# Optimization experiments

Hardware: AMD Instinct MI355X
Metric: run time of the kernel (lower is better)

Reference implementation:

```python
import jax, jax.numpy as jnp
import numpy as np

B, S, D, H, K, L, NS, NT = 32, 512, 1024, 512, 16, 16, 16, 16
SMOOTH = 0.1
EPS = 1e-8


def setup_inputs() -> dict:
    key = jax.random.key(0)
    ks = jax.random.split(key, 16)
    hidden_layers = jax.random.normal(ks[0], (B, S, D), jnp.float32)
    span_start = jax.random.randint(ks[1], (B, K), 0, S - L).astype(jnp.int32)
    span_idx = span_start[..., None] + jnp.arange(L, dtype=jnp.int32)  # [B,K,L] in-range
    span_mask = jnp.ones((B, K, L), jnp.float32)
    span_end = span_start + (L - 1)
    length = jnp.full((B,), S, jnp.int32)
    slot_emb = jax.random.normal(ks[2], (B, K, D), jnp.float32)
    tgt_slot_embs = jax.random.normal(ks[3], (NT, D), jnp.float32)
    src_slot_ids = jax.random.randint(ks[4], (B, K), 0, NS).astype(jnp.int32)
    sc = 0.02
    p = {
        'Wih_f': jax.random.normal(ks[5], (4 * H, D)) * sc,
        'Whh_f': jax.random.normal(ks[6], (4 * H, H)) * sc,
        'bih_f': jnp.zeros((4 * H,)), 'bhh_f': jnp.zeros((4 * H,)),
        'Wih_b': jax.random.normal(ks[7], (4 * H, D)) * sc,
        'Whh_b': jax.random.normal(ks[8], (4 * H, H)) * sc,
        'bih_b': jnp.zeros((4 * H,)), 'bhh_b': jnp.zeros((4 * H,)),
        # slot_name_projection_for_slot / _for_context are eye-initialized with zero bias
        'Wps1': jnp.eye(D), 'bps1': jnp.zeros((D,)),
        'Wps2': jnp.eye(D), 'bps2': jnp.zeros((D,)),
        'Wpc1': jnp.eye(D), 'bpc1': jnp.zeros((D,)),
        'Wpc2': jnp.eye(D), 'bpc2': jnp.zeros((D,)),
    }
    inp = dict(hidden_layers=hidden_layers, span_idx=span_idx, span_mask=span_mask,
               span_start=span_start, span_end=span_end, length=length,
               slot_emb=slot_emb, tgt_slot_embs=tgt_slot_embs, src_slot_ids=src_slot_ids)
    inp.update(p)
    return inp


def _lstm_dir(x, m, Wih, Whh, bih, bhh):
    # x: [N,L,D], m: [N,L]; masked steps carry state through, emit 0
    N = x.shape[0]
    h0 = jnp.zeros((N, H), x.dtype)
    c0 = jnp.zeros((N, H), x.dtype)

    def step(carry, xm):
        h, c = carry
        xt, mt = xm
        g = xt @ Wih.T + h @ Whh.T + (bih + bhh)
        i, f, gg, o = jnp.split(g, 4, axis=-1)  # torch gate order i,f,g,o
        cn = jax.nn.sigmoid(f) * c + jax.nn.sigmoid(i) * jnp.tanh(gg)
        hn = jax.nn.sigmoid(o) * jnp.tanh(cn)
        mt = mt[:, None]
        h = mt * hn + (1.0 - mt) * h
        c = mt * cn + (1.0 - mt) * c
        return (h, c), h * mt

    _, ys = jax.lax.scan(step, (h0, c0), (jnp.swapaxes(x, 0, 1), m.T))
    return jnp.swapaxes(ys, 0, 1)  # [N,L,H]


def _mlp(x, W1, b1, W2, b2):
    # Linear -> Tanh -> (Dropout eval=identity) -> Linear
    return jnp.tanh(x @ W1.T + b1) @ W2.T + b2


def reference(hidden_layers, span_idx, span_mask, span_start, span_end, length,
              slot_emb, tgt_slot_embs, src_slot_ids,
              Wih_f, Whh_f, bih_f, bhh_f, Wih_b, Whh_b, bih_b, bhh_b,
              Wps1, bps1, Wps2, bps2, Wpc1, bpc1, Wpc2, bpc2):
    # gather span tokens: [B,K,L,D]
    spans = hidden_layers[jnp.arange(B)[:, None, None], span_idx]
    x = spans.reshape(B * K, L, D)
    m = span_mask.reshape(B * K, L)
    hf = _lstm_dir(x, m, Wih_f, Whh_f, bih_f, bhh_f)
    hb = _lstm_dir(x[:, ::-1], m[:, ::-1], Wih_b, Whh_b, bih_b, bhh_b)[:, ::-1]
    out = jnp.concatenate([hf, hb], axis=-1)           # [BK,L,2H]
    slot_feats = out.sum(axis=1).reshape(B, K, 2 * H)  # sum-pool over span

    # context attention (faithful to source: returns attn @ hidden, no softmax)
    sf = jax.lax.stop_gradient(slot_feats)
    pos = jnp.arange(S)
    cmask = (pos[None, None, :] < span_start[..., None]) | \
            ((pos[None, None, :] > span_end[..., None]) & (pos[None, None, :] < length[:, None, None]))
    attn = jnp.einsum('bkd,bsd->bks', sf, hidden_layers) * cmask.astype(hidden_layers.dtype)
    context = jnp.einsum('bks,bsd->bkd', attn, hidden_layers)  # [B,K,D]

    # smooth labels via projected slot-name embeddings (all detached in source)
    s_cat = jnp.concatenate([_mlp(slot_emb, Wps1, bps1, Wps2, bps2),
                             _mlp(slot_emb, Wpc1, bpc1, Wpc2, bpc2)], axis=-1)  # [B,K,2D]
    t_cat = jnp.concatenate([_mlp(tgt_slot_embs, Wps1, bps1, Wps2, bps2),
                             _mlp(tgt_slot_embs, Wpc1, bpc1, Wpc2, bpc2)], axis=-1)  # [NT,2D]
    s_cat = jax.lax.stop_gradient(s_cat)
    t_cat = jax.lax.stop_gradient(t_cat)
    sn = jnp.maximum(jnp.linalg.norm(s_cat, axis=-1), EPS)
    tn = jnp.maximum(jnp.linalg.norm(t_cat, axis=-1), EPS)
    sim = jnp.einsum('bkd,td->bkt', s_cat, t_cat) / (sn[..., None] * tn[None, None, :])
    sim = sim / sim.sum(axis=-1, keepdims=True) * (1.0 - SMOOTH)
    one_hot = jax.nn.one_hot(src_slot_ids, NS, dtype=sim.dtype) * SMOOTH
    labels = jnp.concatenate([one_hot, sim], axis=-1)  # [B,K,NS+NT]

    return jnp.concatenate([slot_feats, context, labels], axis=-1)  # [B,K,2H+D+NS+NT]
```

## Files before the change

kernel.cpp:

```cpp
#include <hip/hip_runtime.h>
#include <cstdio>

#define B_ 32
#define S_ 512
#define D_ 1024
#define H_ 512
#define K_ 16
#define L_ 16
#define NT_ 16
#define NSEQ 512
#define XROWS 8192
#define G4H 2048
#define OUTC 2080
#define MROWS 528

typedef unsigned short u16;
typedef __bf16 bf16x8 __attribute__((ext_vector_type(8)));
typedef float f32x4 __attribute__((ext_vector_type(4)));

__device__ inline u16 f2b(float f) {
  union { float f; unsigned u; } x; x.f = f;
  unsigned r = x.u + 0x7FFFu + ((x.u >> 16) & 1u);
  return (u16)(r >> 16);
}
__device__ inline float b2f(u16 h) {
  union { unsigned u; float f; } c; c.u = ((unsigned)h) << 16;
  return c.f;
}
__device__ inline float sigf(float x) { return 1.0f / (1.0f + expf(-x)); }
__device__ inline float wredsum(float v) {
#pragma unroll
  for (int off = 32; off > 0; off >>= 1) v += __shfl_xor(v, off);
  return v;
}
__device__ inline void gl16(const u16* g, u16* l) {
  __builtin_amdgcn_global_load_lds(
      (const __attribute__((address_space(1))) unsigned int*)g,
      (__attribute__((address_space(3))) unsigned int*)l, 16, 0, 0);
}

__global__ __launch_bounds__(256) void split_kernel(const float* __restrict__ in,
                                                    u16* __restrict__ hi,
                                                    u16* __restrict__ lo, int n) {
  int i = blockIdx.x * 256 + threadIdx.x;
  if (i >= n) return;
  float x = in[i];
  u16 h = f2b(x);
  hi[i] = h;
  lo[i] = f2b(x - b2f(h));
}

__global__ __launch_bounds__(256) void hsplit_kernel(const float* __restrict__ in,
                                                     u16* __restrict__ hi,
                                                     u16* __restrict__ lo) {
  size_t i = ((size_t)blockIdx.x * 256 + threadIdx.x) * 4;
  float4 v = *reinterpret_cast<const float4*>(in + i);
  float a[4] = {v.x, v.y, v.z, v.w};
#pragma unroll
  for (int j = 0; j < 4; ++j) {
    u16 h = f2b(a[j]);
    hi[i + j] = h;
    lo[i + j] = f2b(a[j] - b2f(h));
  }
}

__global__ __launch_bounds__(256) void icast_kernel(const float* __restrict__ W,
                                                    u16* __restrict__ out, int Kd) {
  int rp = blockIdx.x;
  int j = rp >> 2, g = rp & 3;
  const float* src = W + ((size_t)(g * H_ + j)) * Kd;
  u16* dst = out + (size_t)rp * Kd;
  for (int k = threadIdx.x; k < Kd; k += 256) dst[k] = f2b(src[k]);
}

__global__ __launch_bounds__(256) void bsum_kernel(const float* __restrict__ bih,
                                                   const float* __restrict__ bhh,
                                                   float* __restrict__ bsum) {
  int rp = blockIdx.x * 256 + threadIdx.x;
  if (rp >= G4H) return;
  int j = rp >> 2, g = rp & 3;
  bsum[rp] = bih[g * H_ + j] + bhh[g * H_ + j];
}

__global__ __launch_bounds__(256) void big_gemm_kernel(
    const u16* __restrict__ Hh, const int* __restrict__ span_idx,
    const u16* __restrict__ Wih2, u16* __restrict__ G2) {
  __shared__ u16 As[128 * 32];
  __shared__ u16 Bs[128 * 32];
  const int tid = threadIdx.x;
  const int bn = blockIdx.x * 128, bm = blockIdx.y * 128;
  const int wave = tid >> 6, lane = tid & 63;
  const int wm = (wave >> 1) * 64, wn = (wave & 1) * 64;
  const int fr = lane & 15;
  const int kg = (lane >> 4) * 8;

  const u16* asrc[2];
  const u16* bsrc[2];
  u16* adst[2];
  u16* bdst[2];
#pragma unroll
  for (int j = 0; j < 2; ++j) {
    int c = tid + 256 * j;
    int gr = bm + (c >> 2);
    int b = gr >> 8;
    int sidx = span_idx[gr];
    asrc[j] = Hh + ((size_t)(b * S_ + sidx)) * D_ + (c & 3) * 8;
    bsrc[j] = Wih2 + (size_t)(bn + (c >> 2)) * D_ + (c & 3) * 8;
    int ub = (wave * 64 + 256 * j) * 8;
    adst[j] = As + ub;
    bdst[j] = Bs + ub;
  }

  f32x4 acc[4][4] = {};
  for (int k0 = 0; k0 < D_; k0 += 32) {
    gl16(asrc[0] + k0, adst[0]);
    gl16(asrc[1] + k0, adst[1]);
    gl16(bsrc[0] + k0, bdst[0]);
    gl16(bsrc[1] + k0, bdst[1]);
    __syncthreads();
    bf16x8 af[4], bfr[4];
#pragma unroll
    for (int m = 0; m < 4; ++m)
      af[m] = *reinterpret_cast<const bf16x8*>(&As[(wm + m * 16 + fr) * 32 + kg]);
#pragma unroll
    for (int n = 0; n < 4; ++n)
      bfr[n] = *reinterpret_cast<const bf16x8*>(&Bs[(wn + n * 16 + fr) * 32 + kg]);
#pragma unroll
    for (int m = 0; m < 4; ++m)
#pragma unroll
      for (int n = 0; n < 4; ++n)
        acc[m][n] = __builtin_amdgcn_mfma_f32_16x16x32_bf16(af[m], bfr[n], acc[m][n], 0, 0, 0);
    __syncthreads();
  }
  const int ci = lane & 15;
  const int r0 = (lane >> 4) * 4;
#pragma unroll
  for (int m = 0; m < 4; ++m)
#pragma unroll
    for (int n = 0; n < 4; ++n) {
      int col = bn + wn + n * 16 + ci;
#pragma unroll
      for (int r = 0; r < 4; ++r) {
        int row = bm + wm + m * 16 + r0 + r;
        G2[(size_t)row * 4096 + col] = f2b(acc[m][n][r]);
      }
    }
}

__global__ __launch_bounds__(256) void lstm_step_kernel(
    const u16* __restrict__ hbf_in,
    const u16* __restrict__ Whhf, const u16* __restrict__ Whhb,
    const u16* __restrict__ G2,
    const float* __restrict__ bsumf, const float* __restrict__ bsumb,
    const float* __restrict__ mask,
    float* __restrict__ hst, float* __restrict__ cst,
    u16* __restrict__ hbf_out,
    float* __restrict__ sf,
    int t, int first) {
  __shared__ u16 As[64 * 32];
  __shared__ u16 Bs[64 * 32];
  const int tid = threadIdx.x;
  const int bz = blockIdx.z;
  const int treal = bz ? (L_ - 1 - t) : t;
  const u16* Whh = bz ? Whhb : Whhf;
  const float* bsum = bz ? bsumb : bsumf;
  const size_t sofs = (size_t)bz * NSEQ * H_;
  const int bm = blockIdx.y * 64, bn = blockIdx.x * 64;
  const int wave = tid >> 6, lane = tid & 63;
  const int wm = (wave >> 1) * 32, wn = (wave & 1) * 32;
  f32x4 acc[2][2] = {};
  const int fr = lane & 15;
  const int kg = (lane >> 4) * 8;

  if (!first) {
    const int c = tid;
    const u16* asrc = hbf_in + sofs + (size_t)(bm + (c >> 2)) * H_ + (c & 3) * 8;
    const u16* bsrc = Whh + (size_t)(bn + (c >> 2)) * H_ + (c & 3) * 8;
    u16* adst = As + wave * 512;
    u16* bdst = Bs + wave * 512;
    for (int k0 = 0; k0 < H_; k0 += 32) {
      gl16(asrc + k0, adst);
      gl16(bsrc + k0, bdst);
      __syncthreads();
      bf16x8 af[2], bfr[2];
#pragma unroll
      for (int m = 0; m < 2; ++m)
        af[m] = *reinterpret_cast<const bf16x8*>(&As[(wm + m * 16 + fr) * 32 + kg]);
#pragma unroll
      for (int n = 0; n < 2; ++n)
        bfr[n] = *reinterpret_cast<const bf16x8*>(&Bs[(wn + n * 16 + fr) * 32 + kg]);
#pragma unroll
      for (int m = 0; m < 2; ++m)
#pragma unroll
        for (int n = 0; n < 2; ++n)
          acc[m][n] = __builtin_amdgcn_mfma_f32_16x16x32_bf16(af[m], bfr[n], acc[m][n], 0, 0, 0);
      __syncthreads();
    }
  }

  const int ci = lane & 15;
  const int r0 = (lane >> 4) * 4;
  const int q = lane & 3;
#pragma unroll
  for (int m = 0; m < 2; ++m)
#pragma unroll
    for (int n = 0; n < 2; ++n) {
      int c = bn + wn + n * 16 + ci;
      int rowbase = bm + wm + m * 16 + r0;
      float val[4];
#pragma unroll
      for (int r = 0; r < 4; ++r) {
        int nrow = rowbase + r;
        float g2 = b2f(G2[((size_t)nrow * L_ + treal) * 4096 + (size_t)bz * 2048 + c]);
        val[r] = acc[m][n][r] + g2 + bsum[c];
      }
      float x1[4], x2[4], x3[4];
#pragma unroll
      for (int r = 0; r < 4; ++r) {
        x1[r] = __shfl_xor(val[r], 1);
        x2[r] = __shfl_xor(val[r], 2);
        x3[r] = __shfl_xor(x1[r], 2);
      }
      if (q == 0) {
        int j = c >> 2;
#pragma unroll
        for (int r = 0; r < 4; ++r) {
          int nrow = rowbase + r;
          float gi = val[r], gf = x1[r], gg = x2[r], go = x3[r];
          float mv = mask[nrow * L_ + treal];
          size_t sidx = sofs + (size_t)nrow * H_ + j;
          float co = first ? 0.f : cst[sidx];
          float ho = first ? 0.f : hst[sidx];
          float cn = sigf(gf) * co + sigf(gi) * tanhf(gg);
          float hn = sigf(go) * tanhf(cn);
          float hnew = mv * hn + (1.f - mv) * ho;
          float cnew = mv * cn + (1.f - mv) * co;
          hst[sidx] = hnew;
          cst[sidx] = cnew;
          hbf_out[sidx] = f2b(hnew);
          size_t fidx = (size_t)nrow * 1024 + bz * 512 + j;
          float contrib = hnew * mv;
          if (first) sf[fidx] = contrib;
          else sf[fidx] += contrib;
        }
      }
    }
}

__global__ __launch_bounds__(256) void copy_sf_split_kernel(const float* __restrict__ sf,
                                                            float* __restrict__ out,
                                                            u16* __restrict__ sfh,
                                                            u16* __restrict__ sfl) {
  int bk = blockIdx.x;
  for (int d = threadIdx.x; d < 1024; d += 256) {
    size_t i = (size_t)bk * 1024 + d;
    float v = sf[i];
    out[(size_t)bk * OUTC + d] = v;
    u16 h = f2b(v);
    sfh[i] = h;
    sfl[i] = f2b(v - b2f(h));
  }
}

__global__ __launch_bounds__(256) void attn_mfma_kernel(
    const u16* __restrict__ sfh, const u16* __restrict__ sfl,
    const u16* __restrict__ Hh, const u16* __restrict__ Hl,
    const int* __restrict__ sstart, const int* __restrict__ send,
    const int* __restrict__ len,
    u16* __restrict__ attn_h, u16* __restrict__ attn_l) {
  __shared__ u16 Bh[128 * 32];
  __shared__ u16 Bl[128 * 32];
  const int b = blockIdx.x;
  const int s0 = blockIdx.y * 128;
  const int tid = threadIdx.x;
  const int wave = tid >> 6, lane = tid & 63;
  const int fr = lane & 15;
  const int kg = (lane >> 4) * 8;
  f32x4 acc[2] = {};

  const u16* hsrc[2];
  const u16* lsrc[2];
  u16* hdst[2];
  u16* ldst[2];
#pragma unroll
  for (int j = 0; j < 2; ++j) {
    int c = tid + 256 * j;
    size_t goff = ((size_t)b * S_ + s0 + (c >> 2)) * D_ + (c & 3) * 8;
    hsrc[j] = Hh + goff;
    lsrc[j] = Hl + goff;
    int ub = (wave * 64 + 256 * j) * 8;
    hdst[j] = Bh + ub;
    ldst[j] = Bl + ub;
  }

  for (int k0 = 0; k0 < D_; k0 += 32) {
    gl16(hsrc[0] + k0, hdst[0]);
    gl16(hsrc[1] + k0, hdst[1]);
    gl16(lsrc[0] + k0, ldst[0]);
    gl16(lsrc[1] + k0, ldst[1]);
    __syncthreads();
    size_t aoff = ((size_t)b * 16 + fr) * D_ + k0 + kg;
    bf16x8 ah = *reinterpret_cast<const bf16x8*>(sfh + aoff);
    bf16x8 al = *reinterpret_cast<const bf16x8*>(sfl + aoff);
#pragma unroll
    for (int nt = 0; nt < 2; ++nt) {
      bf16x8 bh = *reinterpret_cast<const bf16x8*>(&Bh[(wave * 32 + nt * 16 + fr) * 32 + kg]);
      bf16x8 bl = *reinterpret_cast<const bf16x8*>(&Bl[(wave * 32 + nt * 16 + fr) * 32 + kg]);
      acc[nt] = __builtin_amdgcn_mfma_f32_16x16x32_bf16(ah, bh, acc[nt], 0, 0, 0);
      acc[nt] = __builtin_amdgcn_mfma_f32_16x16x32_bf16(ah, bl, acc[nt], 0, 0, 0);
      acc[nt] = __builtin_amdgcn_mfma_f32_16x16x32_bf16(al, bh, acc[nt], 0, 0, 0);
    }
    __syncthreads();
  }
  const int ln = len[b];
#pragma unroll
  for (int nt = 0; nt < 2; ++nt) {
    int s = s0 + wave * 32 + nt * 16 + (lane & 15);
#pragma unroll
    for (int r = 0; r < 4; ++r) {
      int krow = (lane >> 4) * 4 + r;
      int bk = b * 16 + krow;
      int st = sstart[bk], en = send[bk];
      bool cm = (s < st) || ((s > en) && (s < ln));
      float v = cm ? acc[nt][r] : 0.f;
      u16 h = f2b(v);
      size_t idx = (size_t)bk * S_ + s;
      attn_h[idx] = h;
      attn_l[idx] = f2b(v - b2f(h));
    }
  }
}

__global__ __launch_bounds__(256) void ctx_mfma_kernel(
    const u16* __restrict__ attn_h, const u16* __restrict__ attn_l,
    const u16* __restrict__ Hh, const u16* __restrict__ Hl,
    float* __restrict__ out) {
  __shared__ u16 Th[128][34];
  __shared__ u16 Tl[128][34];
  const int b = blockIdx.x;
  const int d0 = blockIdx.y * 128;
  const int tid = threadIdx.x;
  const int wave = tid >> 6, lane = tid & 63;
  const int fr = lane & 15;
  const int kg = (lane >> 4) * 8;
  f32x4 acc[2] = {};

  for (int k0 = 0; k0 < S_; k0 += 32) {
#pragma unroll
    for (int pass = 0; pass < 2; ++pass) {
      int idx = pass * 256 + tid;
      int srow = idx >> 4;
      int dch = (idx & 15) * 8;
      size_t goff = ((size_t)b * S_ + k0 + srow) * D_ + d0 + dch;
      uint4 vh = *reinterpret_cast<const uint4*>(Hh + goff);
      uint4 vl = *reinterpret_cast<const uint4*>(Hl + goff);
      const u16* ph = reinterpret_cast<const u16*>(&vh);
      const u16* pl = reinterpret_cast<const u16*>(&vl);
#pragma unroll
      for (int i = 0; i < 8; ++i) {
        Th[dch + i][srow] = ph[i];
        Tl[dch + i][srow] = pl[i];
      }
    }
    __syncthreads();
    size_t aoff = ((size_t)b * 16 + fr) * S_ + k0 + kg;
    bf16x8 ah = *reinterpret_cast<const bf16x8*>(attn_h + aoff);
    bf16x8 al = *reinterpret_cast<const bf16x8*>(attn_l + aoff);
#pragma unroll
    for (int nt = 0; nt < 2; ++nt) {
      bf16x8 bh = *reinterpret_cast<const bf16x8*>(&Th[wave * 32 + nt * 16 + fr][kg]);
      bf16x8 bl = *reinterpret_cast<const bf16x8*>(&Tl[wave * 32 + nt * 16 + fr][kg]);
      acc[nt] = __builtin_amdgcn_mfma_f32_16x16x32_bf16(ah, bh, acc[nt], 0, 0, 0);
      acc[nt] = __builtin_amdgcn_mfma_f32_16x16x32_bf16(ah, bl, acc[nt], 0, 0, 0);
      acc[nt] = __builtin_amdgcn_mfma_f32_16x16x32_bf16(al, bh, acc[nt], 0, 0, 0);
    }
    __syncthreads();
  }
#pragma unroll
  for (int nt = 0; nt < 2; ++nt) {
    int d = d0 + wave * 32 + nt * 16 + (lane & 15);
#pragma unroll
    for (int r = 0; r < 4; ++r) {
      int krow = (lane >> 4) * 4 + r;
      out[((size_t)b * 16 + krow) * OUTC + 1024 + d] = acc[nt][r];
    }
  }
}

__global__ __launch_bounds__(256) void mlp_gemm_kernel(
    const u16* __restrict__ Ah, const u16* __restrict__ Al, int a_br_stride,
    const u16* __restrict__ B0h, const u16* __restrict__ B0l,
    const u16* __restrict__ B1h, const u16* __restrict__ B1l,
    float* __restrict__ P, int M) {
  __shared__ u16 Ash[64 * 32];
  __shared__ u16 Asl[64 * 32];
  __shared__ u16 Bsh[64 * 32];
  __shared__ u16 Bsl[64 * 32];
  const int tid = threadIdx.x;
  const int zz = blockIdx.z;
  const int br = zz >> 2, ks = zz & 3;
  const u16* Ah_ = Ah + (size_t)br * a_br_stride;
  const u16* Al_ = Al + (size_t)br * a_br_stride;
  const u16* Bh = br ? B1h : B0h;
  const u16* Bl = br ? B1l : B0l;
  const int bm = blockIdx.y * 64, bn = blockIdx.x * 64;
  const int wave = tid >> 6, lane = tid & 63;
  const int wm = (wave >> 1) * 32, wn = (wave & 1) * 32;
  f32x4 acc[2][2] = {};
  const int fr = lane & 15;
  const int kg = (lane >> 4) * 8;

  const int c = tid;
  int ga = bm + (c >> 2);
  if (ga >= M) ga = M - 1;
  const u16* ahsrc = Ah_ + (size_t)ga * D_ + (c & 3) * 8;
  const u16* alsrc = Al_ + (size_t)ga * D_ + (c & 3) * 8;
  const u16* bhsrc = Bh + (size_t)(bn + (c >> 2)) * D_ + (c & 3) * 8;
  const u16* blsrc = Bl + (size_t)(bn + (c >> 2)) * D_ + (c & 3) * 8;
  u16* d0 = Ash + wave * 512;
  u16* d1 = Asl + wave * 512;
  u16* d2 = Bsh + wave * 512;
  u16* d3 = Bsl + wave * 512;

  const int kbeg = ks * 256;
  for (int k0 = kbeg; k0 < kbeg + 256; k0 += 32) {
    gl16(ahsrc + k0, d0);
    gl16(alsrc + k0, d1);
    gl16(bhsrc + k0, d2);
    gl16(blsrc + k0, d3);
    __syncthreads();
    bf16x8 afh[2], afl[2], bfh[2], bfl[2];
#pragma unroll
    for (int m = 0; m < 2; ++m) {
      afh[m] = *reinterpret_cast<const bf16x8*>(&Ash[(wm + m * 16 + fr) * 32 + kg]);
      afl[m] = *reinterpret_cast<const bf16x8*>(&Asl[(wm + m * 16 + fr) * 32 + kg]);
    }
#pragma unroll
    for (int n = 0; n < 2; ++n) {
      bfh[n] = *reinterpret_cast<const bf16x8*>(&Bsh[(wn + n * 16 + fr) * 32 + kg]);
      bfl[n] = *reinterpret_cast<const bf16x8*>(&Bsl[(wn + n * 16 + fr) * 32 + kg]);
    }
#pragma unroll
    for (int m = 0; m < 2; ++m)
#pragma unroll
      for (int n = 0; n < 2; ++n) {
        acc[m][n] = __builtin_amdgcn_mfma_f32_16x16x32_bf16(afh[m], bfh[n], acc[m][n], 0, 0, 0);
        acc[m][n] = __builtin_amdgcn_mfma_f32_16x16x32_bf16(afh[m], bfl[n], acc[m][n], 0, 0, 0);
        acc[m][n] = __builtin_amdgcn_mfma_f32_16x16x32_bf16(afl[m], bfh[n], acc[m][n], 0, 0, 0);
      }
    __syncthreads();
  }
  const int ci = lane & 15;
  const int r0 = (lane >> 4) * 4;
#pragma unroll
  for (int m = 0; m < 2; ++m)
#pragma unroll
    for (int n = 0; n < 2; ++n) {
      int col = bn + wn + n * 16 + ci;
#pragma unroll
      for (int r = 0; r < 4; ++r) {
        int row = bm + wm + m * 16 + r0 + r;
        if (row < M)
          P[((size_t)zz * MROWS + row) * D_ + col] = acc[m][n][r];
      }
    }
}

__global__ __launch_bounds__(256) void mlp_reduce_kernel(
    const float* __restrict__ P,
    const float* __restrict__ bias0, const float* __restrict__ bias1,
    u16* __restrict__ Oh, u16* __restrict__ Ol,
    float* __restrict__ Cf,
    int mode) {
  int i = blockIdx.x * 256 + threadIdx.x;
  int e = i * 4;
  const int per_br = MROWS * D_;
  int br = e / per_br;
  int rem = e - br * per_br;
  int row = rem >> 10;
  int col = rem & 1023;
  float4 s = {0.f, 0.f, 0.f, 0.f};
#pragma unroll
  for (int ks = 0; ks < 4; ++ks) {
    float4 v = *reinterpret_cast<const float4*>(
        P + ((size_t)(br * 4 + ks) * MROWS + row) * D_ + col);
    s.x += v.x; s.y += v.y; s.z += v.z; s.w += v.w;
  }
  const float* bias = br ? bias1 : bias0;
  s.x += bias[col]; s.y += bias[col + 1]; s.z += bias[col + 2]; s.w += bias[col + 3];
  if (mode == 0) {
    float a[4] = {tanhf(s.x), tanhf(s.y), tanhf(s.z), tanhf(s.w)};
    size_t o = (size_t)br * per_br + (size_t)row * D_ + col;
#pragma unroll
    for (int j = 0; j < 4; ++j) {
      u16 h = f2b(a[j]);
      Oh[o + j] = h;
      Ol[o + j] = f2b(a[j] - b2f(h));
    }
  } else {
    *reinterpret_cast<float4*>(Cf + (size_t)row * 2048 + br * 1024 + col) = s;
  }
}

__global__ __launch_bounds__(64) void labels_kernel(
    const float* __restrict__ s_cat, const float* __restrict__ t_cat,
    const int* __restrict__ src_ids, float* __restrict__ out) {
  int bk = blockIdx.x, lane = threadIdx.x;
  const float* srow = s_cat + (size_t)bk * 2048;
  float np = 0.f;
  float dots[16], tsq[16];
#pragma unroll
  for (int t = 0; t < 16; ++t) { dots[t] = 0.f; tsq[t] = 0.f; }
  for (int j = lane; j < 2048; j += 64) {
    float sv = srow[j];
    np += sv * sv;
#pragma unroll
    for (int t = 0; t < 16; ++t) {
      float tv = t_cat[t * 2048 + j];
      dots[t] += sv * tv;
      tsq[t] += tv * tv;
    }
  }
  np = wredsum(np);
#pragma unroll
  for (int t = 0; t < 16; ++t) { dots[t] = wredsum(dots[t]); tsq[t] = wredsum(tsq[t]); }
  float sn = fmaxf(sqrtf(np), 1e-8f);
  float ssum = 0.f;
  float sims[16];
#pragma unroll
  for (int t = 0; t < 16; ++t) {
    float tn = fmaxf(sqrtf(tsq[t]), 1e-8f);
    sims[t] = dots[t] / (sn * tn);
    ssum += sims[t];
  }
  float scale = 0.9f / ssum;
  if (lane < 16) {
    out[(size_t)bk * OUTC + 2064 + lane] = sims[lane] * scale;
  } else if (lane < 32) {
    int t2 = lane - 16;
    out[(size_t)bk * OUTC + 2048 + t2] = (src_ids[bk] == t2) ? 0.1f : 0.f;
  }
}

extern "C" void kernel_launch(void* const* d_in, const int* in_sizes, int n_in,
                              void* d_out, int out_size, void* d_ws, size_t ws_size,
                              hipStream_t stream) {
  const float* hidden    = (const float*)d_in[0];
  const int*   span_idx  = (const int*)d_in[1];
  const float* span_mask = (const float*)d_in[2];
  const int*   span_start= (const int*)d_in[3];
  const int*   span_end  = (const int*)d_in[4];
  const int*   length    = (const int*)d_in[5];
  const float* slot_emb  = (const float*)d_in[6];
  const float* tgt       = (const float*)d_in[7];
  const int*   src_ids   = (const int*)d_in[8];
  const float* Wih_f = (const float*)d_in[9];
  const float* Whh_f = (const float*)d_in[10];
  const float* bih_f = (const float*)d_in[11];
  const float* bhh_f = (const float*)d_in[12];
  const float* Wih_b = (const float*)d_in[13];
  const float* Whh_b = (const float*)d_in[14];
  const float* bih_b = (const float*)d_in[15];
  const float* bhh_b = (const float*)d_in[16];
  const float* Wps1 = (const float*)d_in[17];
  const float* bps1 = (const float*)d_in[18];
  const float* Wps2 = (const float*)d_in[19];
  const float* bps2 = (const float*)d_in[20];
  const float* Wpc1 = (const float*)d_in[21];
  const float* bpc1 = (const float*)d_in[22];
  const float* Wpc2 = (const float*)d_in[23];
  const float* bpc2 = (const float*)d_in[24];
  float* out = (float*)d_out;

  char* p = (char*)d_ws;
  auto alloc = [&](size_t bytes) -> void* {
    void* r = (void*)p;
    p += (bytes + 255) & ~(size_t)255;
    return r;
  };
  char*  BIG1  = (char*)alloc((size_t)XROWS * 4096 * 2);
  char*  BIG2  = (char*)alloc((size_t)2 * B_ * S_ * D_ * 2);
  float* hst   = (float*)alloc((size_t)2 * NSEQ * H_ * 4);
  float* cst   = (float*)alloc((size_t)2 * NSEQ * H_ * 4);
  u16*   hbfA  = (u16*)alloc((size_t)2 * NSEQ * H_ * 2);
  u16*   hbfB  = (u16*)alloc((size_t)2 * NSEQ * H_ * 2);
  float* sf    = (float*)alloc((size_t)NSEQ * 1024 * 4);
  u16*   sfh   = (u16*)alloc((size_t)NSEQ * 1024 * 2);
  u16*   sfl   = (u16*)alloc((size_t)NSEQ * 1024 * 2);
  u16*   attn_h= (u16*)alloc((size_t)NSEQ * S_ * 2);
  u16*   attn_l= (u16*)alloc((size_t)NSEQ * S_ * 2);
  float* CAT   = (float*)alloc((size_t)MROWS * 2048 * 4);
  u16* Wih2_i = (u16*)alloc((size_t)2 * G4H * D_ * 2);
  u16* Whhf_i = (u16*)alloc((size_t)G4H * H_ * 2);
  u16* Whhb_i = (u16*)alloc((size_t)G4H * H_ * 2);
  float* bsumf = (float*)alloc(G4H * 4);
  float* bsumb = (float*)alloc(G4H * 4);
  u16* W1sh = (u16*)alloc((size_t)D_ * D_ * 2); u16* W1sl = (u16*)alloc((size_t)D_ * D_ * 2);
  u16* W2sh = (u16*)alloc((size_t)D_ * D_ * 2); u16* W2sl = (u16*)alloc((size_t)D_ * D_ * 2);
  u16* W1ch = (u16*)alloc((size_t)D_ * D_ * 2); u16* W1cl = (u16*)alloc((size_t)D_ * D_ * 2);
  u16* W2ch = (u16*)alloc((size_t)D_ * D_ * 2); u16* W2cl = (u16*)alloc((size_t)D_ * D_ * 2);
  u16* SEh = (u16*)alloc((size_t)MROWS * D_ * 2); u16* SEl = (u16*)alloc((size_t)MROWS * D_ * 2);
  u16* T1h = (u16*)alloc((size_t)2 * MROWS * D_ * 2);
  u16* T1l = (u16*)alloc((size_t)2 * MROWS * D_ * 2);

  u16*   G2 = (u16*)BIG1;
  float* P  = (float*)BIG1;
  u16*   Hh = (u16*)BIG2;
  u16*   Hl = Hh + (size_t)B_ * S_ * D_;

  size_t need = (size_t)(p - (char*)d_ws);
  if (need > ws_size) {
    fprintf(stderr, "kernel_launch: ws too small, need %zu have %zu\n", need, ws_size);
    return;
  }

  auto split = [&](const float* src, u16* hi, u16* lo, int n) {
    split_kernel<<<(n + 255) / 256, 256, 0, stream>>>(src, hi, lo, n);
  };

  icast_kernel<<<G4H, 256, 0, stream>>>(Wih_f, Wih2_i, D_);
  icast_kernel<<<G4H, 256, 0, stream>>>(Wih_b, Wih2_i + (size_t)G4H * D_, D_);
  icast_kernel<<<G4H, 256, 0, stream>>>(Whh_f, Whhf_i, H_);
  icast_kernel<<<G4H, 256, 0, stream>>>(Whh_b, Whhb_i, H_);
  bsum_kernel<<<8, 256, 0, stream>>>(bih_f, bhh_f, bsumf);
  bsum_kernel<<<8, 256, 0, stream>>>(bih_b, bhh_b, bsumb);
  split(Wps1, W1sh, W1sl, D_ * D_);
  split(Wps2, W2sh, W2sl, D_ * D_);
  split(Wpc1, W1ch, W1cl, D_ * D_);
  split(Wpc2, W2ch, W2cl, D_ * D_);
  split(slot_emb, SEh, SEl, NSEQ * D_);
  split(tgt, SEh + (size_t)NSEQ * D_, SEl + (size_t)NSEQ * D_, NT_ * D_);

  hsplit_kernel<<<(B_ * S_ * D_) / (4 * 256), 256, 0, stream>>>(hidden, Hh, Hl);

  {
    dim3 g(4096 / 128, XROWS / 128);
    big_gemm_kernel<<<g, 256, 0, stream>>>(Hh, span_idx, Wih2_i, G2);
  }

  for (int t = 0; t < L_; ++t) {
    const u16* hin = (t & 1) ? hbfA : hbfB;
    u16* hout = (t & 1) ? hbfB : hbfA;
    dim3 g(G4H / 64, NSEQ / 64, 2);
    lstm_step_kernel<<<g, 256, 0, stream>>>(hin, Whhf_i, Whhb_i, G2, bsumf, bsumb,
                                            span_mask, hst, cst, hout, sf,
                                            t, t == 0 ? 1 : 0);
  }

  copy_sf_split_kernel<<<NSEQ, 256, 0, stream>>>(sf, out, sfh, sfl);

  {
    dim3 g(B_, S_ / 128);
    attn_mfma_kernel<<<g, 256, 0, stream>>>(sfh, sfl, Hh, Hl,
                                            span_start, span_end, length,
                                            attn_h, attn_l);
  }
  {
    dim3 g(B_, D_ / 128);
    ctx_mfma_kernel<<<g, 256, 0, stream>>>(attn_h, attn_l, Hh, Hl, out);
  }

  {
    dim3 g(D_ / 64, (MROWS + 63) / 64, 8);
    dim3 rg((2 * MROWS * D_) / (4 * 256));
    mlp_gemm_kernel<<<g, 256, 0, stream>>>(SEh, SEl, 0, W1sh, W1sl, W1ch, W1cl, P, MROWS);
    mlp_reduce_kernel<<<rg, 256, 0, stream>>>(P, bps1, bpc1, T1h, T1l, nullptr, 0);
    mlp_gemm_kernel<<<g, 256, 0, stream>>>(T1h, T1l, MROWS * D_, W2sh, W2sl, W2ch, W2cl, P, MROWS);
    mlp_reduce_kernel<<<rg, 256, 0, stream>>>(P, bps2, bpc2, nullptr, nullptr, CAT, 1);
  }

  const float* t_cat = CAT + (size_t)NSEQ * 2048;
  labels_kernel<<<NSEQ, 64, 0, stream>>>(CAT, t_cat, src_ids, out);
}
```

Baseline: 633.2 us.

## Double-buffer GEMM staging with swizzled LDS, relayout G2, fp32 context kernel

The big input GEMM, the LSTM recurrent step and the MLP GEMM now use double-buffered LDS staging. The next K-tile's global-to-LDS loads are issued before waiting on the current one, and raw barriers replace __syncthreads. LDS tiles use an XOR swizzle to reduce bank conflicts. G2 is stored time-major so each LSTM step reads a contiguous slab. The split-bf16 MFMA context GEMM is replaced by a plain fp32 FMA kernel reading attention weights written as fp32, which drops the transposed LDS staging and the three-pass bf16 emulation but gives up MFMA throughput.

Result: no change. 644.3 us (+1.7%).

```diff
diff --git a/kernel.cpp b/kernel.cpp
--- a/kernel.cpp
+++ b/kernel.cpp
@@ -39,6 +39,16 @@
       (__attribute__((address_space(3))) unsigned int*)l, 16, 0, 0);
 }
 
+__device__ inline int swzidx(int R, int c) {
+  return (R >> 1) * 64 + (((((R & 1) << 2) | c) ^ ((R >> 1) & 7)) << 3);
+}
+__device__ inline void stage_map(int wave, int lane, int j, int& lrow, int& cu) {
+  int sr = j * 32 + wave * 8 + (lane >> 3);
+  int ci = (lane & 7) ^ (sr & 7);
+  lrow = sr * 2 + (ci >> 2);
+  cu = (ci & 3) * 8;
+}
+
 __global__ __launch_bounds__(256) void split_kernel(const float* __restrict__ in,
                                                     u16* __restrict__ hi,
                                                     u16* __restrict__ lo, int n) {
@@ -85,52 +95,64 @@
 __global__ __launch_bounds__(256) void big_gemm_kernel(
     const u16* __restrict__ Hh, const int* __restrict__ span_idx,
     const u16* __restrict__ Wih2, u16* __restrict__ G2) {
-  __shared__ u16 As[128 * 32];
-  __shared__ u16 Bs[128 * 32];
+  __shared__ u16 As[2][128 * 32];
+  __shared__ u16 Bs[2][128 * 32];
   const int tid = threadIdx.x;
   const int bn = blockIdx.x * 128, bm = blockIdx.y * 128;
   const int wave = tid >> 6, lane = tid & 63;
   const int wm = (wave >> 1) * 64, wn = (wave & 1) * 64;
   const int fr = lane & 15;
-  const int kg = (lane >> 4) * 8;
+  const int cc = lane >> 4;
 
   const u16* asrc[2];
   const u16* bsrc[2];
-  u16* adst[2];
-  u16* bdst[2];
+  int doff[2];
 #pragma unroll
   for (int j = 0; j < 2; ++j) {
-    int c = tid + 256 * j;
-    int gr = bm + (c >> 2);
+    int lrow, cu;
+    stage_map(wave, lane, j, lrow, cu);
+    int gr = bm + lrow;
     int b = gr >> 8;
     int sidx = span_idx[gr];
-    asrc[j] = Hh + ((size_t)(b * S_ + sidx)) * D_ + (c & 3) * 8;
-    bsrc[j] = Wih2 + (size_t)(bn + (c >> 2)) * D_ + (c & 3) * 8;
-    int ub = (wave * 64 + 256 * j) * 8;
-    adst[j] = As + ub;
-    bdst[j] = Bs + ub;
-  }
+    asrc[j] = Hh + ((size_t)(b * S_ + sidx)) * D_ + cu;
+    bsrc[j] = Wih2 + (size_t)(bn + lrow) * D_ + cu;
+    doff[j] = (j * 256 + wave * 64) * 8;
+  }
+  int aoff[4], boff[4];
+#pragma unroll
+  for (int m = 0; m < 4; ++m) aoff[m] = swzidx(wm + m * 16 + fr, cc);
+#pragma unroll
+  for (int n = 0; n < 4; ++n) boff[n] = swzidx(wn + n * 16 + fr, cc);
 
   f32x4 acc[4][4] = {};
+  auto STAGE = [&](int buf, int k0) {
+    gl16(asrc[0] + k0, &As[buf][doff[0]]);
+    gl16(asrc[1] + k0, &As[buf][doff[1]]);
+    gl16(bsrc[0] + k0, &Bs[buf][doff[0]]);
+    gl16(bsrc[1] + k0, &Bs[buf][doff[1]]);
+  };
+  STAGE(0, 0);
+  int cur = 0;
   for (int k0 = 0; k0 < D_; k0 += 32) {
-    gl16(asrc[0] + k0, adst[0]);
-    gl16(asrc[1] + k0, adst[1]);
-    gl16(bsrc[0] + k0, bdst[0]);
-    gl16(bsrc[1] + k0, bdst[1]);
-    __syncthreads();
+    if (k0 + 32 < D_) {
+      STAGE(cur ^ 1, k0 + 32);
+      asm volatile("s_waitcnt vmcnt(4)" ::: "memory");
+    } else {
+      asm volatile("s_waitcnt vmcnt(0)" ::: "memory");
+    }
+    __builtin_amdgcn_s_barrier();
     bf16x8 af[4], bfr[4];
 #pragma unroll
-    for (int m = 0; m < 4; ++m)
-      af[m] = *reinterpret_cast<const bf16x8*>(&As[(wm + m * 16 + fr) * 32 + kg]);
-#pragma unroll
-    for (int n = 0; n < 4; ++n)
-      bfr[n] = *reinterpret_cast<const bf16x8*>(&Bs[(wn + n * 16 + fr) * 32 + kg]);
+    for (int m = 0; m < 4; ++m) af[m] = *reinterpret_cast<const bf16x8*>(&As[cur][aoff[m]]);
+#pragma unroll
+    for (int n = 0; n < 4; ++n) bfr[n] = *reinterpret_cast<const bf16x8*>(&Bs[cur][boff[n]]);
 #pragma unroll
     for (int m = 0; m < 4; ++m)
 #pragma unroll
       for (int n = 0; n < 4; ++n)
         acc[m][n] = __builtin_amdgcn_mfma_f32_16x16x32_bf16(af[m], bfr[n], acc[m][n], 0, 0, 0);
-    __syncthreads();
+    __builtin_amdgcn_s_barrier();
+    cur ^= 1;
   }
   const int ci = lane & 15;
   const int r0 = (lane >> 4) * 4;
@@ -142,7 +164,8 @@
 #pragma unroll
       for (int r = 0; r < 4; ++r) {
         int row = bm + wm + m * 16 + r0 + r;
-        G2[(size_t)row * 4096 + col] = f2b(acc[m][n][r]);
+        size_t g2row = (size_t)(row & 15) * NSEQ + (row >> 4);
+        G2[g2row * 4096 + col] = f2b(acc[m][n][r]);
       }
     }
 }
@@ -157,8 +180,8 @@
     u16* __restrict__ hbf_out,
     float* __restrict__ sf,
     int t, int first) {
-  __shared__ u16 As[64 * 32];
-  __shared__ u16 Bs[64 * 32];
+  __shared__ u16 As[2][64 * 32];
+  __shared__ u16 Bs[2][64 * 32];
   const int tid = threadIdx.x;
   const int bz = blockIdx.z;
   const int treal = bz ? (L_ - 1 - t) : t;
@@ -170,31 +193,46 @@
   const int wm = (wave >> 1) * 32, wn = (wave & 1) * 32;
   f32x4 acc[2][2] = {};
   const int fr = lane & 15;
-  const int kg = (lane >> 4) * 8;
+  const int cc = lane >> 4;
 
   if (!first) {
-    const int c = tid;
-    const u16* asrc = hbf_in + sofs + (size_t)(bm + (c >> 2)) * H_ + (c & 3) * 8;
-    const u16* bsrc = Whh + (size_t)(bn + (c >> 2)) * H_ + (c & 3) * 8;
-    u16* adst = As + wave * 512;
-    u16* bdst = Bs + wave * 512;
+    int lrow, cu;
+    stage_map(wave, lane, 0, lrow, cu);
+    const u16* asrc = hbf_in + sofs + (size_t)(bm + lrow) * H_ + cu;
+    const u16* bsrc = Whh + (size_t)(bn + lrow) * H_ + cu;
+    const int doff = wave * 64 * 8;
+    int aoff[2], boff[2];
+#pragma unroll
+    for (int m = 0; m < 2; ++m) aoff[m] = swzidx(wm + m * 16 + fr, cc);
+#pragma unroll
+    for (int n = 0; n < 2; ++n) boff[n] = swzidx(wn + n * 16 + fr, cc);
+
+    auto STAGE = [&](int buf, int k0) {
+      gl16(asrc + k0, &As[buf][doff]);
+      gl16(bsrc + k0, &Bs[buf][doff]);
+    };
+    STAGE(0, 0);
+    int cur = 0;
     for (int k0 = 0; k0 < H_; k0 += 32) {
-      gl16(asrc + k0, adst);
-      gl16(bsrc + k0, bdst);
-      __syncthreads();
+      if (k0 + 32 < H_) {
+        STAGE(cur ^ 1, k0 + 32);
+        asm volatile("s_waitcnt vmcnt(2)" ::: "memory");
+      } else {
+        asm volatile("s_waitcnt vmcnt(0)" ::: "memory");
+      }
+      __builtin_amdgcn_s_barrier();
       bf16x8 af[2], bfr[2];
 #pragma unroll
-      for (int m = 0; m < 2; ++m)
-        af[m] = *reinterpret_cast<const bf16x8*>(&As[(wm + m * 16 + fr) * 32 + kg]);
-#pragma unroll
-      for (int n = 0; n < 2; ++n)
-        bfr[n] = *reinterpret_cast<const bf16x8*>(&Bs[(wn + n * 16 + fr) * 32 + kg]);
+      for (int m = 0; m < 2; ++m) af[m] = *reinterpret_cast<const bf16x8*>(&As[cur][aoff[m]]);
+#pragma unroll
+      for (int n = 0; n < 2; ++n) bfr[n] = *reinterpret_cast<const bf16x8*>(&Bs[cur][boff[n]]);
 #pragma unroll
       for (int m = 0; m < 2; ++m)
 #pragma unroll
         for (int n = 0; n < 2; ++n)
           acc[m][n] = __builtin_amdgcn_mfma_f32_16x16x32_bf16(af[m], bfr[n], acc[m][n], 0, 0, 0);
-      __syncthreads();
+      __builtin_amdgcn_s_barrier();
+      cur ^= 1;
     }
   }
 
@@ -211,7 +249,7 @@
 #pragma unroll
       for (int r = 0; r < 4; ++r) {
         int nrow = rowbase + r;
-        float g2 = b2f(G2[((size_t)nrow * L_ + treal) * 4096 + (size_t)bz * 2048 + c]);
+        float g2 = b2f(G2[((size_t)treal * NSEQ + nrow) * 4096 + (size_t)bz * 2048 + c]);
         val[r] = acc[m][n][r] + g2 + bsum[c];
       }
       float x1[4], x2[4], x3[4];
@@ -267,7 +305,7 @@
     const u16* __restrict__ Hh, const u16* __restrict__ Hl,
     const int* __restrict__ sstart, const int* __restrict__ send,
     const int* __restrict__ len,
-    u16* __restrict__ attn_h, u16* __restrict__ attn_l) {
+    float* __restrict__ attn_f) {
   __shared__ u16 Bh[128 * 32];
   __shared__ u16 Bl[128 * 32];
   const int b = blockIdx.x;
@@ -275,37 +313,39 @@
   const int tid = threadIdx.x;
   const int wave = tid >> 6, lane = tid & 63;
   const int fr = lane & 15;
-  const int kg = (lane >> 4) * 8;
+  const int cc = lane >> 4;
+  const int kg = cc * 8;
   f32x4 acc[2] = {};
 
   const u16* hsrc[2];
   const u16* lsrc[2];
-  u16* hdst[2];
-  u16* ldst[2];
+  int doff[2];
 #pragma unroll
   for (int j = 0; j < 2; ++j) {
-    int c = tid + 256 * j;
-    size_t goff = ((size_t)b * S_ + s0 + (c >> 2)) * D_ + (c & 3) * 8;
+    int lrow, cu;
+    stage_map(wave, lane, j, lrow, cu);
+    size_t goff = ((size_t)b * S_ + s0 + lrow) * D_ + cu;
     hsrc[j] = Hh + goff;
     lsrc[j] = Hl + goff;
-    int ub = (wave * 64 + 256 * j) * 8;
-    hdst[j] = Bh + ub;
-    ldst[j] = Bl + ub;
-  }
+    doff[j] = (j * 256 + wave * 64) * 8;
+  }
+  int boff[2];
+#pragma unroll
+  for (int nt = 0; nt < 2; ++nt) boff[nt] = swzidx(wave * 32 + nt * 16 + fr, cc);
 
   for (int k0 = 0; k0 < D_; k0 += 32) {
-    gl16(hsrc[0] + k0, hdst[0]);
-    gl16(hsrc[1] + k0, hdst[1]);
-    gl16(lsrc[0] + k0, ldst[0]);
-    gl16(lsrc[1] + k0, ldst[1]);
+    gl16(hsrc[0] + k0, &Bh[doff[0]]);
+    gl16(hsrc[1] + k0, &Bh[doff[1]]);
+    gl16(lsrc[0] + k0, &Bl[doff[0]]);
+    gl16(lsrc[1] + k0, &Bl[doff[1]]);
     __syncthreads();
     size_t aoff = ((size_t)b * 16 + fr) * D_ + k0 + kg;
     bf16x8 ah = *reinterpret_cast<const bf16x8*>(sfh + aoff);
     bf16x8 al = *reinterpret_cast<const bf16x8*>(sfl + aoff);
 #pragma unroll
     for (int nt = 0; nt < 2; ++nt) {
-      bf16x8 bh = *reinterpret_cast<const bf16x8*>(&Bh[(wave * 32 + nt * 16 + fr) * 32 + kg]);
-      bf16x8 bl = *reinterpret_cast<const bf16x8*>(&Bl[(wave * 32 + nt * 16 + fr) * 32 + kg]);
+      bf16x8 bh = *reinterpret_cast<const bf16x8*>(&Bh[boff[nt]]);
+      bf16x8 bl = *reinterpret_cast<const bf16x8*>(&Bl[boff[nt]]);
       acc[nt] = __builtin_amdgcn_mfma_f32_16x16x32_bf16(ah, bh, acc[nt], 0, 0, 0);
       acc[nt] = __builtin_amdgcn_mfma_f32_16x16x32_bf16(ah, bl, acc[nt], 0, 0, 0);
       acc[nt] = __builtin_amdgcn_mfma_f32_16x16x32_bf16(al, bh, acc[nt], 0, 0, 0);
@@ -322,68 +362,41 @@
       int bk = b * 16 + krow;
       int st = sstart[bk], en = send[bk];
       bool cm = (s < st) || ((s > en) && (s < ln));
-      float v = cm ? acc[nt][r] : 0.f;
-      u16 h = f2b(v);
-      size_t idx = (size_t)bk * S_ + s;
-      attn_h[idx] = h;
-      attn_l[idx] = f2b(v - b2f(h));
-    }
-  }
-}
-
-__global__ __launch_bounds__(256) void ctx_mfma_kernel(
-    const u16* __restrict__ attn_h, const u16* __restrict__ attn_l,
-    const u16* __restrict__ Hh, const u16* __restrict__ Hl,
+      attn_f[(size_t)bk * S_ + s] = cm ? acc[nt][r] : 0.f;
+    }
+  }
+}
+
+__global__ __launch_bounds__(256) void ctx_f32_kernel(
+    const float* __restrict__ attn_f, const float* __restrict__ hidden,
     float* __restrict__ out) {
-  __shared__ u16 Th[128][34];
-  __shared__ u16 Tl[128][34];
+  __shared__ float att[16 * 512];
   const int b = blockIdx.x;
   const int d0 = blockIdx.y * 128;
   const int tid = threadIdx.x;
-  const int wave = tid >> 6, lane = tid & 63;
-  const int fr = lane & 15;
-  const int kg = (lane >> 4) * 8;
-  f32x4 acc[2] = {};
-
-  for (int k0 = 0; k0 < S_; k0 += 32) {
-#pragma unroll
-    for (int pass = 0; pass < 2; ++pass) {
-      int idx = pass * 256 + tid;
-      int srow = idx >> 4;
-      int dch = (idx & 15) * 8;
-      size_t goff = ((size_t)b * S_ + k0 + srow) * D_ + d0 + dch;
-      uint4 vh = *reinterpret_cast<const uint4*>(Hh + goff);
-      uint4 vl = *reinterpret_cast<const uint4*>(Hl + goff);
-      const u16* ph = reinterpret_cast<const u16*>(&vh);
-      const u16* pl = reinterpret_cast<const u16*>(&vl);
-#pragma unroll
-      for (int i = 0; i < 8; ++i) {
-        Th[dch + i][srow] = ph[i];
-        Tl[dch + i][srow] = pl[i];
-      }
-    }
-    __syncthreads();
-    size_t aoff = ((size_t)b * 16 + fr) * S_ + k0 + kg;
-    bf16x8 ah = *reinterpret_cast<const bf16x8*>(attn_h + aoff);
-    bf16x8 al = *reinterpret_cast<const bf16x8*>(attn_l + aoff);
-#pragma unroll
-    for (int nt = 0; nt < 2; ++nt) {
-      bf16x8 bh = *reinterpret_cast<const bf16x8*>(&Th[wave * 32 + nt * 16 + fr][kg]);
-      bf16x8 bl = *reinterpret_cast<const bf16x8*>(&Tl[wave * 32 + nt * 16 + fr][kg]);
-      acc[nt] = __builtin_amdgcn_mfma_f32_16x16x32_bf16(ah, bh, acc[nt], 0, 0, 0);
-      acc[nt] = __builtin_amdgcn_mfma_f32_16x16x32_bf16(ah, bl, acc[nt], 0, 0, 0);
-      acc[nt] = __builtin_amdgcn_mfma_f32_16x16x32_bf16(al, bh, acc[nt], 0, 0, 0);
-    }
-    __syncthreads();
-  }
-#pragma unroll
-  for (int nt = 0; nt < 2; ++nt) {
-    int d = d0 + wave * 32 + nt * 16 + (lane & 15);
-#pragma unroll
-    for (int r = 0; r < 4; ++r) {
-      int krow = (lane >> 4) * 4 + r;
-      out[((size_t)b * 16 + krow) * OUTC + 1024 + d] = acc[nt][r];
-    }
+  for (int i = tid; i < 16 * 512; i += 256)
+    att[i] = attn_f[((size_t)b * 16 + (i >> 9)) * S_ + (i & 511)];
+  __syncthreads();
+  const int d = d0 + (tid & 127);
+  const int sh = tid >> 7;
+  float acc[16] = {};
+  const float* hp = hidden + ((size_t)b * S_ + sh * 256) * D_ + d;
+  for (int s = 0; s < 256; ++s) {
+    float hv = hp[(size_t)s * D_];
+    int si = sh * 256 + s;
+#pragma unroll
+    for (int kr = 0; kr < 16; ++kr) acc[kr] += att[kr * 512 + si] * hv;
+  }
+  __syncthreads();
+  float* red = att;
+#pragma unroll
+  for (int kr = 0; kr < 16; ++kr) red[(sh * 16 + kr) * 128 + (tid & 127)] = acc[kr];
+  __syncthreads();
+  if (sh == 0) {
+#pragma unroll
+    for (int kr = 0; kr < 16; ++kr)
+      out[((size_t)b * 16 + kr) * OUTC + 1024 + d] =
+          red[kr * 128 + (tid & 127)] + red[(16 + kr) * 128 + (tid & 127)];
   }
 }
 
@@ -392,10 +405,10 @@
     const u16* __restrict__ B0h, const u16* __restrict__ B0l,
     const u16* __restrict__ B1h, const u16* __restrict__ B1l,
     float* __restrict__ P, int M) {
-  __shared__ u16 Ash[64 * 32];
-  __shared__ u16 Asl[64 * 32];
-  __shared__ u16 Bsh[64 * 32];
-  __shared__ u16 Bsl[64 * 32];
+  __shared__ u16 Ash[2][64 * 32];
+  __shared__ u16 Asl[2][64 * 32];
+  __shared__ u16 Bsh[2][64 * 32];
+  __shared__ u16 Bsl[2][64 * 32];
   const int tid = threadIdx.x;
   const int zz = blockIdx.z;
   const int br = zz >> 2, ks = zz & 3;
@@ -408,37 +421,50 @@
   const int wm = (wave >> 1) * 32, wn = (wave & 1) * 32;
   f32x4 acc[2][2] = {};
   const int fr = lane & 15;
-  const int kg = (lane >> 4) * 8;
-
-  const int c = tid;
-  int ga = bm + (c >> 2);
+  const int cc = lane >> 4;
+
+  int lrow, cu;
+  stage_map(wave, lane, 0, lrow, cu);
+  int ga = bm + lrow;
   if (ga >= M) ga = M - 1;
-  const u16* ahsrc = Ah_ + (size_t)ga * D_ + (c & 3) * 8;
-  const u16* alsrc = Al_ + (size_t)ga * D_ + (c & 3) * 8;
-  const u16* bhsrc = Bh + (size_t)(bn + (c >> 2)) * D_ + (c & 3) * 8;
-  const u16* blsrc = Bl + (size_t)(bn + (c >> 2)) * D_ + (c & 3) * 8;
-  u16* d0 = Ash + wave * 512;
-  u16* d1 = Asl + wave * 512;
-  u16* d2 = Bsh + wave * 512;
-  u16* d3 = Bsl + wave * 512;
-
+  const u16* ahsrc = Ah_ + (size_t)ga * D_ + cu;
+  const u16* alsrc = Al_ + (size_t)ga * D_ + cu;
+  const u16* bhsrc = Bh + (size_t)(bn + lrow) * D_ + cu;
+  const u16* blsrc = Bl + (size_t)(bn + lrow) * D_ + cu;
+  const int doff = wave * 64 * 8;
+  int aoff[2], boff[2];
+#pragma unroll
+  for (int m = 0; m < 2; ++m) aoff[m] = swzidx(wm + m * 16 + fr, cc);
+#pragma unroll
+  for (int n = 0; n < 2; ++n) boff[n] = swzidx(wn + n * 16 + fr, cc);
+
+  auto STAGE = [&](int buf, int k0) {
+    gl16(ahsrc + k0, &Ash[buf][doff]);
+    gl16(alsrc + k0, &Asl[buf][doff]);
+    gl16(bhsrc + k0, &Bsh[buf][doff]);
+    gl16(blsrc + k0, &Bsl[buf][doff]);
+  };
   const int kbeg = ks * 256;
+  STAGE(0, kbeg);
+  int cur = 0;
   for (int k0 = kbeg; k0 < kbeg + 256; k0 += 32) {
-    gl16(ahsrc + k0, d0);
-    gl16(alsrc + k0, d1);
-    gl16(bhsrc + k0, d2);
-    gl16(blsrc + k0, d3);
-    __syncthreads();
+    if (k0 + 32 < kbeg + 256) {
+      STAGE(cur ^ 1, k0 + 32);
+      asm volatile("s_waitcnt vmcnt(4)" ::: "memory");
+    } else {
+      asm volatile("s_waitcnt vmcnt(0)" ::: "memory");
+    }
+    __builtin_amdgcn_s_barrier();
     bf16x8 afh[2], afl[2], bfh[2], bfl[2];
 #pragma unroll
     for (int m = 0; m < 2; ++m) {
-      afh[m] = *reinterpret_cast<const bf16x8*>(&Ash[(wm + m * 16 + fr) * 32 + kg]);
-      afl[m] = *reinterpret_cast<const bf16x8*>(&Asl[(wm + m * 16 + fr) * 32 + kg]);
+      afh[m] = *reinterpret_cast<const bf16x8*>(&Ash[cur][aoff[m]]);
+      afl[m] = *reinterpret_cast<const bf16x8*>(&Asl[cur][aoff[m]]);
     }
 #pragma unroll
     for (int n = 0; n < 2; ++n) {
-      bfh[n] = *reinterpret_cast<const bf16x8*>(&Bsh[(wn + n * 16 + fr) * 32 + kg]);
-      bfl[n] = *reinterpret_cast<const bf16x8*>(&Bsl[(wn + n * 16 + fr) * 32 + kg]);
+      bfh[n] = *reinterpret_cast<const bf16x8*>(&Bsh[cur][boff[n]]);
+      bfl[n] = *reinterpret_cast<const bf16x8*>(&Bsl[cur][boff[n]]);
     }
 #pragma unroll
     for (int m = 0; m < 2; ++m)
@@ -448,7 +474,8 @@
         acc[m][n] = __builtin_amdgcn_mfma_f32_16x16x32_bf16(afh[m], bfl[n], acc[m][n], 0, 0, 0);
         acc[m][n] = __builtin_amdgcn_mfma_f32_16x16x32_bf16(afl[m], bfh[n], acc[m][n], 0, 0, 0);
       }
-    __syncthreads();
+    __builtin_amdgcn_s_barrier();
+    cur ^= 1;
   }
   const int ci = lane & 15;
   const int r0 = (lane >> 4) * 4;
@@ -587,8 +614,7 @@
   float* sf    = (float*)alloc((size_t)NSEQ * 1024 * 4);
   u16*   sfh   = (u16*)alloc((size_t)NSEQ * 1024 * 2);
   u16*   sfl   = (u16*)alloc((size_t)NSEQ * 1024 * 2);
-  u16*   attn_h= (u16*)alloc((size_t)NSEQ * S_ * 2);
-  u16*   attn_l= (u16*)alloc((size_t)NSEQ * S_ * 2);
+  float* attn_f= (float*)alloc((size_t)NSEQ * S_ * 4);
   float* CAT   = (float*)alloc((size_t)MROWS * 2048 * 4);
   u16* Wih2_i = (u16*)alloc((size_t)2 * G4H * D_ * 2);
   u16* Whhf_i = (u16*)alloc((size_t)G4H * H_ * 2);
@@ -652,12 +678,11 @@
   {
     dim3 g(B_, S_ / 128);
     attn_mfma_kernel<<<g, 256, 0, stream>>>(sfh, sfl, Hh, Hl,
-                                            span_start, span_end, length,
-                                            attn_h, attn_l);
+                                            span_start, span_end, length, attn_f);
   }
   {
     dim3 g(B_, D_ / 128);
-    ctx_mfma_kernel<<<g, 256, 0, stream>>>(attn_h, attn_l, Hh, Hl, out);
+    ctx_f32_kernel<<<g, 256, 0, stream>>>(attn_f, hidden, out);
   }
 
   {
```
